# Optimization experiments

Measured on AMD Instinct MI355X. Metric: run time of the kernel, lower is better.

The kernel has to match this reference:

```python
import jax, jax.numpy as jnp
import numpy as np

EPS = 1e-8

def _layernorm(x, gamma, beta):
    # torch-style: std with Bessel correction (ddof=1), eps added to std
    D = x.shape[-1]
    mean = jnp.mean(x, axis=-1, keepdims=True)
    var = jnp.sum((x - mean) ** 2, axis=-1, keepdims=True) / (D - 1)
    std = jnp.sqrt(var)
    return (x - mean) / (std + EPS) * gamma + beta


def setup_inputs() -> dict:
    key = jax.random.key(0)
    B, T, D, H = 1, 2048, 1024, 16
    Dh = D // H
    ks = jax.random.split(key, 8)
    s = 0.02
    return {
        "x": jax.random.normal(ks[0], (B, T, D), jnp.float32),
        "wq": jax.random.normal(ks[1], (H, D, Dh), jnp.float32) * s,
        "wk": jax.random.normal(ks[2], (H, D, Dh), jnp.float32) * s,
        "wv": jax.random.normal(ks[3], (H, D, Dh), jnp.float32) * s,
        "wo": jax.random.normal(ks[4], (D, D), jnp.float32) * s,
        "bo": jnp.zeros((D,), jnp.float32),
        "ln1_g": jnp.ones((D,), jnp.float32),
        "ln1_b": jnp.zeros((D,), jnp.float32),
        "ln2_g": jnp.ones((D,), jnp.float32),
        "ln2_b": jnp.zeros((D,), jnp.float32),
        "w1": jax.random.normal(ks[5], (D, 4 * D), jnp.float32) * s,
        "b1": jnp.zeros((4 * D,), jnp.float32),
        "w2": jax.random.normal(ks[6], (4 * D, D), jnp.float32) * s,
        "b2": jnp.zeros((D,), jnp.float32),
    }


def reference(x, wq, wk, wv, wo, bo, ln1_g, ln1_b, ln2_g, ln2_b, w1, b1, w2, b2):
    B, T, D = x.shape
    H, _, Dh = wq.shape
    # --- attention sublayer (dropout p used at eval => identity) ---
    h = _layernorm(x, ln1_g, ln1_b)
    q = jnp.einsum('btd,hde->bhte', h, wq)
    k = jnp.einsum('btd,hde->bhte', h, wk)
    v = jnp.einsum('btd,hde->bhte', h, wv)
    scores = jnp.einsum('bhte,bhse->bhts', q, k) / jnp.sqrt(jnp.float32(Dh))
    causal = jnp.triu(jnp.ones((T, T), bool), 1)  # True above diagonal => masked
    scores = jnp.where(causal, -jnp.inf, scores)
    attn = jax.nn.softmax(scores, axis=-1)
    ctx = jnp.einsum('bhts,bhse->bthe', attn, v).reshape(B, T, H * Dh)
    att_out = ctx @ wo + bo
    x = x + att_out
    # --- FFN sublayer ---
    h2 = _layernorm(x, ln2_g, ln2_b)
    ffn = jax.nn.gelu(h2 @ w1 + b1, approximate=False) @ w2 + b2
    return x + ffn
```

## Files before the change

### kernel.cpp

```cpp
#include <hip/hip_runtime.h>
#include <hip/hip_bf16.h>
#include <math.h>

typedef unsigned short bf16u;
typedef __attribute__((ext_vector_type(8))) short short8;
typedef __attribute__((ext_vector_type(4))) float floatx4;

__device__ __forceinline__ float bf2f(bf16u u) {
  union { unsigned int i; float f; } c;
  c.i = ((unsigned int)u) << 16;
  return c.f;
}
__device__ __forceinline__ bf16u f2bf(float f) {
  union { float f; unsigned int i; } c;
  c.f = f;
  unsigned int lsb = (c.i >> 16) & 1u;
  c.i += 0x7fffu + lsb;
  return (bf16u)(c.i >> 16);
}

__device__ __forceinline__ void load_lds16(const void* g, void* l) {
  __builtin_amdgcn_global_load_lds(
      (const __attribute__((address_space(1))) void*)g,
      (__attribute__((address_space(3))) void*)l, 16, 0, 0);
}

__global__ __launch_bounds__(256) void ln_kernel(
    const float* __restrict__ x, bf16u* __restrict__ out,
    const float* __restrict__ gamma, const float* __restrict__ beta) {
  const int row = blockIdx.x;
  const int tid = threadIdx.x;
  const int lane = tid & 63, wave = tid >> 6;
  __shared__ float red[4];
  const float* xr = x + (size_t)row * 1024;
  float v[4];
#pragma unroll
  for (int i = 0; i < 4; i++) v[i] = xr[tid + i * 256];
  float s = v[0] + v[1] + v[2] + v[3];
#pragma unroll
  for (int off = 32; off; off >>= 1) s += __shfl_down(s, off);
  if (lane == 0) red[wave] = s;
  __syncthreads();
  const float mean = (red[0] + red[1] + red[2] + red[3]) * (1.0f / 1024.0f);
  __syncthreads();
  float sq = 0.f;
#pragma unroll
  for (int i = 0; i < 4; i++) { float d = v[i] - mean; sq += d * d; }
#pragma unroll
  for (int off = 32; off; off >>= 1) sq += __shfl_down(sq, off);
  if (lane == 0) red[wave] = sq;
  __syncthreads();
  const float var = (red[0] + red[1] + red[2] + red[3]) * (1.0f / 1023.0f);
  const float inv = 1.0f / (sqrtf(var) + 1e-8f);
  bf16u* orow = out + (size_t)row * 1024;
#pragma unroll
  for (int i = 0; i < 4; i++) {
    int idx = tid + i * 256;
    orow[idx] = f2bf((v[i] - mean) * inv * gamma[idx] + beta[idx]);
  }
}

__global__ __launch_bounds__(256) void pack_weights(
    const float* __restrict__ wq, const float* __restrict__ wk,
    const float* __restrict__ wv, const float* __restrict__ wo,
    const float* __restrict__ w1, const float* __restrict__ w2,
    bf16u* __restrict__ WqkvT, bf16u* __restrict__ woT,
    bf16u* __restrict__ w1T, bf16u* __restrict__ w2T) {
  __shared__ bf16u tile[32][33];
  const int id = blockIdx.x;
  const float* in; bf16u* out; int R, C, bx, by;
  if (id < 3072) {
    int job = id >> 10, rem = id & 1023;
    int head = rem >> 6, t = rem & 63;
    bx = t & 1; by = t >> 1;
    in = (job == 0 ? wq : (job == 1 ? wk : wv)) + head * 65536;
    out = WqkvT + job * 1048576 + head * 65536;
    R = 1024; C = 64;
  } else if (id < 4096) {
    int rem = id - 3072; bx = rem & 31; by = rem >> 5;
    in = wo; out = woT; R = 1024; C = 1024;
  } else if (id < 8192) {
    int rem = id - 4096; bx = rem & 127; by = rem >> 7;
    in = w1; out = w1T; R = 1024; C = 4096;
  } else {
    int rem = id - 8192; bx = rem & 31; by = rem >> 5;
    in = w2; out = w2T; R = 4096; C = 1024;
  }
  const int bc = bx * 32, br = by * 32;
  const int lx = threadIdx.x & 31, ly = threadIdx.x >> 5;
#pragma unroll
  for (int i = 0; i < 32; i += 8)
    tile[ly + i][lx] = f2bf(in[(size_t)(br + ly + i) * C + bc + lx]);
  __syncthreads();
#pragma unroll
  for (int i = 0; i < 32; i += 8)
    out[(size_t)(bc + ly + i) * R + br + lx] = tile[lx][ly + i];
}

__global__ __launch_bounds__(256) void transpose_b(
    const bf16u* __restrict__ in, bf16u* __restrict__ out,
    int ins, int coff, int outs) {
  __shared__ bf16u tile[32][33];
  const int bc = blockIdx.x * 32, br = blockIdx.y * 32;
  const int lx = threadIdx.x & 31, ly = threadIdx.x >> 5;
#pragma unroll
  for (int i = 0; i < 32; i += 8)
    tile[ly + i][lx] = in[(size_t)(br + ly + i) * ins + coff + bc + lx];
  __syncthreads();
#pragma unroll
  for (int i = 0; i < 32; i += 8)
    out[(size_t)(bc + ly + i) * outs + br + lx] = tile[lx][ly + i];
}

template <int BM, int BN, int WGR, int WGC, int EPI>
__global__ __launch_bounds__(256, (BN == 128 ? 2 : 4)) void gemm_bt(
    const bf16u* __restrict__ A, const bf16u* __restrict__ Bt,
    const float* __restrict__ bias, const float* __restrict__ res,
    void* __restrict__ Cout, int M, int N, int K, int kchunk) {
  constexpr int BK = 64;
  constexpr int TM = BM / WGR, TN = BN / WGC;
  constexpr int NI = TM / 16, NJ = TN / 16;
  alignas(16) __shared__ bf16u sA[BM * BK];
  alignas(16) __shared__ bf16u sB[BN * BK];
  const int tid = threadIdx.x, lane = tid & 63, wave = tid >> 6;
  const int wr = wave / WGC, wc = wave % WGC;
  const int quad = lane >> 4, l16 = lane & 15;
  const int m0 = blockIdx.y * BM, n0 = blockIdx.x * BN;
  const int kz = blockIdx.z;
  const int kbeg = kz * kchunk;
  const int kend = (kbeg + kchunk < K) ? (kbeg + kchunk) : K;

  floatx4 acc[NI][NJ] = {};
  constexpr int ACH = BM * BK / 8;
  constexpr int BCH = BN * BK / 8;

  for (int k0 = kbeg; k0 < kend; k0 += BK) {
#pragma unroll
    for (int c = tid; c < ACH; c += 256) {
      int r = c >> 3, kc = ((c ^ r) & 7) * 8;
      load_lds16(A + (size_t)(m0 + r) * K + k0 + kc, (void*)(sA + c * 8));
    }
#pragma unroll
    for (int c = tid; c < BCH; c += 256) {
      int r = c >> 3, kc = ((c ^ r) & 7) * 8;
      load_lds16(Bt + (size_t)(n0 + r) * K + k0 + kc, (void*)(sB + c * 8));
    }
    __syncthreads();
#pragma unroll
    for (int kk = 0; kk < BK; kk += 32) {
      const int ch = (kk >> 3) + quad;
      short8 af[NI], bf[NJ];
#pragma unroll
      for (int i = 0; i < NI; i++) {
        const int R = wr * TM + i * 16 + l16;
        af[i] = *(const short8*)(sA + R * BK + ((ch ^ (R & 7)) << 3));
      }
#pragma unroll
      for (int j = 0; j < NJ; j++) {
        const int R = wc * TN + j * 16 + l16;
        bf[j] = *(const short8*)(sB + R * BK + ((ch ^ (R & 7)) << 3));
      }
#pragma unroll
      for (int i = 0; i < NI; i++)
#pragma unroll
        for (int j = 0; j < NJ; j++)
          acc[i][j] = __builtin_amdgcn_mfma_f32_16x16x32_bf16(af[i], bf[j], acc[i][j], 0, 0, 0);
    }
    __syncthreads();
  }

  float* pout = (float*)Cout;
  if constexpr (EPI == 3) pout += (size_t)kz * M * N;
#pragma unroll
  for (int j = 0; j < NJ; j++) {
    const int col = n0 + wc * TN + j * 16 + l16;
    float bv = 0.0f;
    if constexpr (EPI == 1 || EPI == 2) bv = bias[col];
#pragma unroll
    for (int i = 0; i < NI; i++) {
#pragma unroll
      for (int r = 0; r < 4; r++) {
        const int row = m0 + wr * TM + i * 16 + quad * 4 + r;
        const size_t o = (size_t)row * N + col;
        const float v = acc[i][j][r];
        if constexpr (EPI == 0) {
          ((bf16u*)Cout)[o] = f2bf(v);
        } else if constexpr (EPI == 1) {
          pout[o] = v + bv + res[o];
        } else if constexpr (EPI == 2) {
          float t = v + bv;
          ((bf16u*)Cout)[o] = f2bf(0.5f * t * (1.0f + erff(t * 0.70710678118654752f)));
        } else {
          pout[o] = v;
        }
      }
    }
  }
}

__global__ __launch_bounds__(256) void reduce2_kernel(
    const float* __restrict__ part, const float* __restrict__ bias,
    const float* __restrict__ res, float* __restrict__ out,
    int N, size_t total) {
  size_t i = ((size_t)blockIdx.x * 256 + threadIdx.x) * 4;
  if (i >= total) return;
  float4 a = *(const float4*)(part + i);
  float4 b = *(const float4*)(part + total + i);
  float4 r = *(const float4*)(res + i);
  float4 bv = *(const float4*)(bias + (int)(i & (size_t)(N - 1)));
  float4 o;
  o.x = a.x + b.x + r.x + bv.x;
  o.y = a.y + b.y + r.y + bv.y;
  o.z = a.z + b.z + r.z + bv.z;
  o.w = a.w + b.w + r.w + bv.w;
  *(float4*)(out + i) = o;
}

template <int NT>
__device__ __forceinline__ void attn_tile(
    const bf16u* sQ, const bf16u* sK, const bf16u* sVt, bf16u* sP,
    floatx4* aco, floatx4& acc_l, short8 ones,
    int q0, int c0, int wave, int quad, int l16) {
  constexpr int SK = 72, SV = 136;
  floatx4 s[NT] = {};
#pragma unroll
  for (int kk = 0; kk < 64; kk += 32) {
    short8 aq = *(const short8*)(sQ + (wave * 16 + l16) * SK + kk + quad * 8);
#pragma unroll
    for (int nt = 0; nt < NT; nt++) {
      short8 bk = *(const short8*)(sK + (nt * 16 + l16) * SK + kk + quad * 8);
      s[nt] = __builtin_amdgcn_mfma_f32_16x16x32_bf16(bk, aq, s[nt], 0, 0, 0);
    }
  }
  const float C = 0.125f * 1.44269504088896f;
  const int qrow = q0 + wave * 16 + l16;
#pragma unroll
  for (int nt = 0; nt < NT; nt++)
#pragma unroll
    for (int r = 0; r < 4; r++) {
      const int kpos = c0 + nt * 16 + quad * 4 + r;
      float t = s[nt][r] * C;
      if (kpos > qrow) t = -__builtin_inff();
      s[nt][r] = __builtin_amdgcn_exp2f(t);
    }
  __syncthreads();
#pragma unroll
  for (int nt = 0; nt < NT; nt++) {
    unsigned int lo = (unsigned int)f2bf(s[nt][0]) | ((unsigned int)f2bf(s[nt][1]) << 16);
    unsigned int hi = (unsigned int)f2bf(s[nt][2]) | ((unsigned int)f2bf(s[nt][3]) << 16);
    uint2 pk; pk.x = lo; pk.y = hi;
    *(uint2*)(sP + (wave * 16 + l16) * SV + nt * 16 + quad * 4) = pk;
  }
  __syncthreads();
#pragma unroll
  for (int kk = 0; kk < NT * 16; kk += 32) {
    short8 ap = *(const short8*)(sP + (wave * 16 + l16) * SV + kk + quad * 8);
#pragma unroll
    for (int dt = 0; dt < 4; dt++) {
      short8 bv = *(const short8*)(sVt + (dt * 16 + l16) * SV + kk + quad * 8);
      aco[dt] = __builtin_amdgcn_mfma_f32_16x16x32_bf16(ap, bv, aco[dt], 0, 0, 0);
    }
    acc_l = __builtin_amdgcn_mfma_f32_16x16x32_bf16(ap, ones, acc_l, 0, 0, 0);
  }
}

template <int NZ>
__global__ __launch_bounds__(256, 3) void flash_attn(
    const bf16u* __restrict__ QKV, const bf16u* __restrict__ Vt,
    bf16u* __restrict__ partO, float* __restrict__ partL) {
  const int qb = 31 - blockIdx.x;
  const int h = blockIdx.y;
  const int z = blockIdx.z;
  const int tid = threadIdx.x, lane = tid & 63, wave = tid >> 6;
  const int quad = lane >> 4, l16 = lane & 15;
  constexpr int SK = 72, SV = 136;
  alignas(16) __shared__ bf16u sQ[64 * SK];
  alignas(16) __shared__ bf16u sK[128 * SK];
  alignas(16) __shared__ bf16u sVt[64 * SV];
  bf16u* sP = sK;
  const int q0 = qb * 64;

  for (int c = tid; c < 512; c += 256) {
    int r = c >> 3, e8 = (c & 7) * 8;
    *(uint4*)(sQ + r * SK + e8) =
        *(const uint4*)(QKV + (size_t)(q0 + r) * 3072 + h * 64 + e8);
  }

  floatx4 acc_l = {0.f, 0.f, 0.f, 0.f};
  floatx4 aco[4] = {};
  short8 ones;
#pragma unroll
  for (int u = 0; u < 8; u++) ones[u] = (short)0x3F80;

  const int nkt = (qb >> 1) + 1;
  for (int kt = z; kt < nkt; kt += NZ) {
    const int c0 = kt * 128;
    __syncthreads();
    for (int c = tid; c < 1024; c += 256) {
      int r = c >> 3, e8 = (c & 7) * 8;
      *(uint4*)(sK + r * SK + e8) =
          *(const uint4*)(QKV + (size_t)(c0 + r) * 3072 + 1024 + h * 64 + e8);
    }
    for (int c = tid; c < 1024; c += 256) {
      int e = c >> 4, s8 = (c & 15) * 8;
      *(uint4*)(sVt + e * SV + s8) =
          *(const uint4*)(Vt + (size_t)(h * 64 + e) * 2048 + c0 + s8);
    }
    __syncthreads();
    if (kt == nkt - 1 && (qb & 1) == 0)
      attn_tile<4>(sQ, sK, sVt, sP, aco, acc_l, ones, q0, c0, wave, quad, l16);
    else
      attn_tile<8>(sQ, sK, sVt, sP, aco, acc_l, ones, q0, c0, wave, quad, l16);
  }
  bf16u* po = partO + ((size_t)z * 2048 + q0) * 1024 + h * 64;
#pragma unroll
  for (int dt = 0; dt < 4; dt++)
#pragma unroll
    for (int r = 0; r < 4; r++)
      po[(wave * 16 + quad * 4 + r) * 1024 + dt * 16 + l16] = f2bf(aco[dt][r]);
  if (l16 == 0) {
#pragma unroll
    for (int r = 0; r < 4; r++)
      partL[((size_t)z * 2048 + q0 + wave * 16 + quad * 4 + r) * 16 + h] = acc_l[r];
  }
}

template <int NZ>
__global__ __launch_bounds__(256) void attn_reduce(
    const bf16u* __restrict__ partO, const float* __restrict__ partL,
    bf16u* __restrict__ ctx) {
  const int t = blockIdx.x;
  const int col = threadIdx.x * 4;
  const int h = col >> 6;
  float l = 0.f;
#pragma unroll
  for (int z = 0; z < NZ; z++) l += partL[((size_t)z * 2048 + t) * 16 + h];
  float o0 = 0.f, o1 = 0.f, o2 = 0.f, o3 = 0.f;
#pragma unroll
  for (int z = 0; z < NZ; z++) {
    uint2 v = *(const uint2*)(partO + ((size_t)z * 2048 + t) * 1024 + col);
    o0 += bf2f((bf16u)(v.x & 0xffff)); o1 += bf2f((bf16u)(v.x >> 16));
    o2 += bf2f((bf16u)(v.y & 0xffff)); o3 += bf2f((bf16u)(v.y >> 16));
  }
  const float inv = 1.0f / l;
  uint2 pk;
  pk.x = (unsigned int)f2bf(o0 * inv) | ((unsigned int)f2bf(o1 * inv) << 16);
  pk.y = (unsigned int)f2bf(o2 * inv) | ((unsigned int)f2bf(o3 * inv) << 16);
  *(uint2*)(ctx + (size_t)t * 1024 + col) = pk;
}

extern "C" void kernel_launch(void* const* d_in, const int* in_sizes, int n_in,
                              void* d_out, int out_size, void* d_ws, size_t ws_size,
                              hipStream_t stream) {
  (void)in_sizes; (void)n_in; (void)out_size; (void)ws_size;
  const float* x   = (const float*)d_in[0];
  const float* wq  = (const float*)d_in[1];
  const float* wk  = (const float*)d_in[2];
  const float* wv  = (const float*)d_in[3];
  const float* wo  = (const float*)d_in[4];
  const float* bo  = (const float*)d_in[5];
  const float* g1  = (const float*)d_in[6];
  const float* be1 = (const float*)d_in[7];
  const float* g2  = (const float*)d_in[8];
  const float* be2 = (const float*)d_in[9];
  const float* w1  = (const float*)d_in[10];
  const float* bb1 = (const float*)d_in[11];
  const float* w2  = (const float*)d_in[12];
  const float* bb2 = (const float*)d_in[13];

  char* p = (char*)d_ws;
  const size_t MB = 1024 * 1024;
  constexpr int NZ = 4;
  bf16u* WqkvT = (bf16u*)(p + 0 * MB);
  bf16u* woT   = (bf16u*)(p + 6 * MB);
  bf16u* w1T   = (bf16u*)(p + 8 * MB);
  bf16u* w2T   = (bf16u*)(p + 16 * MB);
  bf16u* multi = (bf16u*)(p + 24 * MB);
  bf16u* QKV   = (bf16u*)(p + 28 * MB);
  float* partL = (float*)(p + 40 * MB);
  bf16u* partO = (bf16u*)(p + 41 * MB);
  bf16u* mid   = (bf16u*)(p + 28 * MB);
  float* x1    = (float*)(p + 49 * MB);
  float* partF = (float*)(p + 0 * MB);
  bf16u* hln = multi, *Vtr = multi, *ctx = multi, *h2 = multi;

  pack_weights<<<12288, 256, 0, stream>>>(wq, wk, wv, wo, w1, w2,
                                          WqkvT, woT, w1T, w2T);

  ln_kernel<<<2048, 256, 0, stream>>>(x, hln, g1, be1);
  gemm_bt<64, 128, 2, 2, 0><<<dim3(24, 32, 1), 256, 0, stream>>>(
      hln, WqkvT, nullptr, nullptr, QKV, 2048, 3072, 1024, 1024);
  transpose_b<<<dim3(32, 64), 256, 0, stream>>>(QKV, Vtr, 3072, 2048, 2048);
  flash_attn<NZ><<<dim3(32, 16, NZ), 256, 0, stream>>>(QKV, Vtr, partO, partL);
  attn_reduce<NZ><<<2048, 256, 0, stream>>>(partO, partL, ctx);
  gemm_bt<32, 64, 2, 2, 1><<<dim3(16, 64, 1), 256, 0, stream>>>(
      ctx, woT, bo, x, x1, 2048, 1024, 1024, 1024);
  ln_kernel<<<2048, 256, 0, stream>>>(x1, h2, g2, be2);
  gemm_bt<64, 128, 2, 2, 2><<<dim3(32, 32, 1), 256, 0, stream>>>(
      h2, w1T, bb1, nullptr, mid, 2048, 4096, 1024, 1024);
  gemm_bt<64, 64, 2, 2, 3><<<dim3(16, 32, 2), 256, 0, stream>>>(
      mid, w2T, nullptr, nullptr, partF, 2048, 1024, 4096, 2048);
  reduce2_kernel<<<2048, 256, 0, stream>>>(partF, bb2, x1, (float*)d_out,
                                           1024, (size_t)2048 * 1024);
}
```

Before: 288.6 us.

## Swizzle attention LDS tiles, skip causal mask on interior tiles, raise occupancy

Replaces the padded shared-memory layouts for Q, K, V-transpose and P in the attention kernel with XOR-swizzled unpadded layouts. This cuts LDS footprint and is meant to avoid bank conflicts on the 16-byte loads. The causal mask is now applied only on the diagonal tile via a template flag, which removes compare-and-select work from interior tiles. Launch bounds rise to 4 blocks per SM for both the attention kernel and all GEMM variants, which risks register spills in the 128-wide GEMM.

Result: faster. 272.2 us (-5.7%).

```diff
diff --git a/kernel.cpp b/kernel.cpp
--- a/kernel.cpp
+++ b/kernel.cpp
@@ -113,7 +113,7 @@
 }
 
 template <int BM, int BN, int WGR, int WGC, int EPI>
-__global__ __launch_bounds__(256, (BN == 128 ? 2 : 4)) void gemm_bt(
+__global__ __launch_bounds__(256, 4) void gemm_bt(
     const bf16u* __restrict__ A, const bf16u* __restrict__ Bt,
     const float* __restrict__ bias, const float* __restrict__ res,
     void* __restrict__ Cout, int M, int N, int K, int kchunk) {
@@ -216,31 +216,35 @@
   *(float4*)(out + i) = o;
 }
 
-template <int NT>
+template <int NT, bool MASK>
 __device__ __forceinline__ void attn_tile(
     const bf16u* sQ, const bf16u* sK, const bf16u* sVt, bf16u* sP,
     floatx4* aco, floatx4& acc_l, short8 ones,
     int q0, int c0, int wave, int quad, int l16) {
-  constexpr int SK = 72, SV = 136;
+  const int rq = wave * 16 + l16;
   floatx4 s[NT] = {};
 #pragma unroll
   for (int kk = 0; kk < 64; kk += 32) {
-    short8 aq = *(const short8*)(sQ + (wave * 16 + l16) * SK + kk + quad * 8);
+    const int ch = (kk >> 3) + quad;
+    short8 aq = *(const short8*)(sQ + rq * 64 + ((ch ^ (rq & 7)) << 3));
 #pragma unroll
     for (int nt = 0; nt < NT; nt++) {
-      short8 bk = *(const short8*)(sK + (nt * 16 + l16) * SK + kk + quad * 8);
+      const int rk = nt * 16 + l16;
+      short8 bk = *(const short8*)(sK + rk * 64 + ((ch ^ (rk & 7)) << 3));
       s[nt] = __builtin_amdgcn_mfma_f32_16x16x32_bf16(bk, aq, s[nt], 0, 0, 0);
     }
   }
   const float C = 0.125f * 1.44269504088896f;
-  const int qrow = q0 + wave * 16 + l16;
+  const int qrow = q0 + rq;
 #pragma unroll
   for (int nt = 0; nt < NT; nt++)
 #pragma unroll
     for (int r = 0; r < 4; r++) {
-      const int kpos = c0 + nt * 16 + quad * 4 + r;
       float t = s[nt][r] * C;
-      if (kpos > qrow) t = -__builtin_inff();
+      if constexpr (MASK) {
+        const int kpos = c0 + nt * 16 + quad * 4 + r;
+        if (kpos > qrow) t = -__builtin_inff();
+      }
       s[nt][r] = __builtin_amdgcn_exp2f(t);
     }
   __syncthreads();
@@ -249,15 +253,19 @@
     unsigned int lo = (unsigned int)f2bf(s[nt][0]) | ((unsigned int)f2bf(s[nt][1]) << 16);
     unsigned int hi = (unsigned int)f2bf(s[nt][2]) | ((unsigned int)f2bf(s[nt][3]) << 16);
     uint2 pk; pk.x = lo; pk.y = hi;
-    *(uint2*)(sP + (wave * 16 + l16) * SV + nt * 16 + quad * 4) = pk;
+    const int e0 = nt * 16 + quad * 4;
+    const int cch = e0 >> 3, sub = e0 & 7;
+    *(uint2*)(sP + rq * 128 + ((cch ^ (rq & 7)) << 3) + sub) = pk;
   }
   __syncthreads();
 #pragma unroll
   for (int kk = 0; kk < NT * 16; kk += 32) {
-    short8 ap = *(const short8*)(sP + (wave * 16 + l16) * SV + kk + quad * 8);
+    const int ch = (kk >> 3) + quad;
+    short8 ap = *(const short8*)(sP + rq * 128 + ((ch ^ (rq & 7)) << 3));
 #pragma unroll
     for (int dt = 0; dt < 4; dt++) {
-      short8 bv = *(const short8*)(sVt + (dt * 16 + l16) * SV + kk + quad * 8);
+      const int rv = dt * 16 + l16;
+      short8 bv = *(const short8*)(sVt + rv * 128 + ((ch ^ (rv & 7)) << 3));
       aco[dt] = __builtin_amdgcn_mfma_f32_16x16x32_bf16(ap, bv, aco[dt], 0, 0, 0);
     }
     acc_l = __builtin_amdgcn_mfma_f32_16x16x32_bf16(ap, ones, acc_l, 0, 0, 0);
@@ -265,7 +273,7 @@
 }
 
 template <int NZ>
-__global__ __launch_bounds__(256, 3) void flash_attn(
+__global__ __launch_bounds__(256, 4) void flash_attn(
     const bf16u* __restrict__ QKV, const bf16u* __restrict__ Vt,
     bf16u* __restrict__ partO, float* __restrict__ partL) {
   const int qb = 31 - blockIdx.x;
@@ -273,17 +281,16 @@
   const int z = blockIdx.z;
   const int tid = threadIdx.x, lane = tid & 63, wave = tid >> 6;
   const int quad = lane >> 4, l16 = lane & 15;
-  constexpr int SK = 72, SV = 136;
-  alignas(16) __shared__ bf16u sQ[64 * SK];
-  alignas(16) __shared__ bf16u sK[128 * SK];
-  alignas(16) __shared__ bf16u sVt[64 * SV];
+  alignas(16) __shared__ bf16u sQ[64 * 64];
+  alignas(16) __shared__ bf16u sK[128 * 64];
+  alignas(16) __shared__ bf16u sVt[64 * 128];
   bf16u* sP = sK;
   const int q0 = qb * 64;
 
   for (int c = tid; c < 512; c += 256) {
-    int r = c >> 3, e8 = (c & 7) * 8;
-    *(uint4*)(sQ + r * SK + e8) =
-        *(const uint4*)(QKV + (size_t)(q0 + r) * 3072 + h * 64 + e8);
+    int r = c >> 3, cc = c & 7;
+    *(uint4*)(sQ + r * 64 + ((cc ^ (r & 7)) << 3)) =
+        *(const uint4*)(QKV + (size_t)(q0 + r) * 3072 + h * 64 + cc * 8);
   }
 
   floatx4 acc_l = {0.f, 0.f, 0.f, 0.f};
@@ -297,20 +304,24 @@
     const int c0 = kt * 128;
     __syncthreads();
     for (int c = tid; c < 1024; c += 256) {
-      int r = c >> 3, e8 = (c & 7) * 8;
-      *(uint4*)(sK + r * SK + e8) =
-          *(const uint4*)(QKV + (size_t)(c0 + r) * 3072 + 1024 + h * 64 + e8);
+      int r = c >> 3, cc = c & 7;
+      *(uint4*)(sK + r * 64 + ((cc ^ (r & 7)) << 3)) =
+          *(const uint4*)(QKV + (size_t)(c0 + r) * 3072 + 1024 + h * 64 + cc * 8);
     }
     for (int c = tid; c < 1024; c += 256) {
-      int e = c >> 4, s8 = (c & 15) * 8;
-      *(uint4*)(sVt + e * SV + s8) =
-          *(const uint4*)(Vt + (size_t)(h * 64 + e) * 2048 + c0 + s8);
+      int e = c >> 4, cc = c & 15;
+      *(uint4*)(sVt + e * 128 + ((cc ^ (e & 7)) << 3)) =
+          *(const uint4*)(Vt + (size_t)(h * 64 + e) * 2048 + c0 + cc * 8);
     }
     __syncthreads();
-    if (kt == nkt - 1 && (qb & 1) == 0)
-      attn_tile<4>(sQ, sK, sVt, sP, aco, acc_l, ones, q0, c0, wave, quad, l16);
-    else
-      attn_tile<8>(sQ, sK, sVt, sP, aco, acc_l, ones, q0, c0, wave, quad, l16);
+    if (kt == nkt - 1) {
+      if ((qb & 1) == 0)
+        attn_tile<4, true>(sQ, sK, sVt, sP, aco, acc_l, ones, q0, c0, wave, quad, l16);
+      else
+        attn_tile<8, true>(sQ, sK, sVt, sP, aco, acc_l, ones, q0, c0, wave, quad, l16);
+    } else {
+      attn_tile<8, false>(sQ, sK, sVt, sP, aco, acc_l, ones, q0, c0, wave, quad, l16);
+    }
   }
   bf16u* po = partO + ((size_t)z * 2048 + q0) * 1024 + h * 64;
 #pragma unroll
```
